# Optimization experiments

Measured on AMD Instinct MI355X. Metric: run time of the kernel, lower is better.

The kernel has to match this reference:

```python
import jax, jax.numpy as jnp
import numpy as np

ITERS = 2
EPS = 1e-6

_OFFSETS = [(a, b, c) for a in (-1, 0, 1) for b in (-1, 0, 1) for c in (-1, 0, 1)]


def _erosion_step(im):
    # product over full 3x3x3 neighborhood (connectivity=26 -> all 27 voxels),
    # out-of-bounds padded with 1 (identity for product)
    B, C, D, H, W = im.shape
    p = jnp.pad(im, ((0, 0), (0, 0), (1, 1), (1, 1), (1, 1)), constant_values=1.0)
    prod = jnp.ones_like(im)
    for dz, dy, dx in _OFFSETS:
        prod = prod * p[:, :, 1 + dz:1 + dz + D, 1 + dy:1 + dy + H, 1 + dx:1 + dx + W]
    return prod


def _distance_map(im, iters=ITERS):
    # PositiveDistanceMap: dils = -SoftErosion3D(1-im) where SoftErosion3D
    # returns temp = -sum_k im_k (im_0 = 1-im, im_{k+1} = im_k * erosion(im_k))
    cur = 1.0 - im
    acc = jnp.zeros_like(cur)
    for _ in range(iters):
        acc = acc + cur
        cur = cur * _erosion_step(cur)
    return acc


def _lah_loss(x, y_onehot):
    axes = (2, 3, 4)  # batch_lah=False -> per (batch, class) reduction
    dm_hat = _distance_map(x)
    dm_gt = _distance_map(y_onehot)
    fp = (dm_gt * x).sum(axes)
    fn = (dm_hat * y_onehot).sum(axes)
    # norm == 0
    fp = fp / (x.sum(axes) + EPS)
    fn = fn / (y_onehot.sum(axes) + EPS)
    lah = (fp + fn + jnp.abs(fp - fn)) / 2  # logsum2 == elementwise max
    return lah[:, 1:].mean()  # do_bg=False drops background channel


def setup_inputs() -> dict:
    key = jax.random.key(0)
    k1, k2 = jax.random.split(key)
    x = jax.random.uniform(k1, (2, 4, 128, 128, 128), dtype=jnp.float32)
    y = jax.random.randint(k2, (2, 1, 128, 128, 128), 0, 4, dtype=jnp.int64)
    return {"x": x, "y": y}


def reference(x, y):
    C = x.shape[1]
    y_onehot = jax.nn.one_hot(y[:, 0], C, axis=1, dtype=x.dtype)  # [B,C,D,H,W]
    return _lah_loss(x, y_onehot)
```

## Files before the change

kernel.cpp:

```cpp
#include <hip/hip_runtime.h>

constexpr int SPB = 1 << 21;
constexpr float EPSV = 1e-6f;

__device__ unsigned char g_mask[2 * SPB];

constexpr int K0_ZSEG = 4;
constexpr int K0_NBLK = (2 * (128 / K0_ZSEG) * 128) / 4;

struct MEnt { int pk, cx, cy; };

__device__ __forceinline__ MEnt k0_load(const int* __restrict__ yb, int s,
                                        int rbase0, bool ym1, bool yp1) {
    MEnt e;
    const int rb = (s << 14) | rbase0;
    int2 vc = *(const int2*)(yb + rb);
    int nib0 = 1 << vc.x, nib1 = 1 << vc.y;
    if (ym1) { int2 vm = *(const int2*)(yb + rb - 128); nib0 |= 1 << vm.x; nib1 |= 1 << vm.y; }
    if (yp1) { int2 vp = *(const int2*)(yb + rb + 128); nib0 |= 1 << vp.x; nib1 |= 1 << vp.y; }
    e.pk = nib0 | (nib1 << 8);
    e.cx = vc.x; e.cy = vc.y;
    return e;
}

__global__ __launch_bounds__(256) void mask_build(const int* __restrict__ y32) {
    const int wid = (blockIdx.x << 2) | (threadIdx.x >> 6);
    const int lane = threadIdx.x & 63;
    const int yy = wid & 127;
    const int zs = (wid >> 7) & 31;
    const int b = (wid >> 12) & 1;
    const int x0 = lane << 1;
    const int z0 = zs * K0_ZSEG;
    const bool ym1 = yy > 0, yp1 = yy < 127;
    const int rbase0 = (yy << 7) | x0;

    const int* __restrict__ yb = y32 + ((long)b << 21);
    unsigned char* __restrict__ mb = g_mask + ((long)b << 21);

    MEnt e0, e1;
    if (z0 > 0) e0 = k0_load(yb, z0 - 1, rbase0, ym1, yp1);
    else { e0.pk = 0; e0.cx = 0; e0.cy = 0; }
    e1 = k0_load(yb, z0, rbase0, ym1, yp1);

#pragma unroll
    for (int dz = 0; dz < K0_ZSEG; ++dz) {
        const int z = z0 + dz;
        MEnt e2;
        if (z + 1 < 128) e2 = k0_load(yb, z + 1, rbase0, ym1, yp1);
        else { e2.pk = 0; e2.cx = 0; e2.cy = 0; }

        const int zor = e0.pk | e1.pk | e2.pk;
        int orL = __shfl_up(zor, 1);
        if (lane == 0) orL = 0;
        int orR = __shfl_down(zor, 1);
        if (lane == 63) orR = 0;
        const int full0 = (zor | (zor >> 8) | (orL >> 8)) & 15;
        const int full1 = (zor | (zor >> 8) | orR) & 15;

        const unsigned short st =
            (unsigned short)((full0 | (e1.cx << 4)) | ((full1 | (e1.cy << 4)) << 8));
        *(unsigned short*)(mb + ((z << 14) | rbase0)) = st;

        e0 = e1; e1 = e2;
    }
}

constexpr int ZC = 8;
constexpr int NBLK = 8 * 16 * (128 / ZC);

__global__ __launch_bounds__(256) void lah_main(const float* __restrict__ x,
                                                float* __restrict__ ws) {
    __shared__ float lds[4][2][4][128];
    __shared__ float sred[4];

    float* acc = ws;
    const float* zp = ws + 64;

    const int bid = blockIdx.x;
    const int plane = bid & 7;
    const int b = plane >> 2, cls = plane & 3;
    const int inner = bid >> 3;
    const int quad = inner & 15;
    const int zq = inner >> 4;
    const int t = threadIdx.x;
    const int w = t >> 6;
    const int rp = quad * 4 + w;
    const int lane = t & 63;
    const int hf = lane >> 5;
    const int lx = lane & 31;
    const int xc = lx << 2;
    const int z0 = zq * ZC;

    const int rowA = 2 * rp - 1 + hf;
    const int rowB = 2 * rp + 1 + hf;
    const int rout = 2 * rp + hf;
    const bool okA = rowA >= 0;
    const bool okB = rowB <= 127;
    const int offA = (rowA << 7) + xc;
    const int offB = (rowB << 7) + xc;

    const float* __restrict__ xp = x + ((long)plane << 21);
    const unsigned char* __restrict__ mb = g_mask + ((long)b << 21);

    auto stage = [&](int k, bool want) {
        const int sl = k & 1;
        const bool kOK = want && ((unsigned)k < 128u);
        const float* pa = (kOK && okA) ? (xp + (k << 14) + offA) : zp;
        const float* pb = (kOK && okB) ? (xp + (k << 14) + offB) : zp;
        __builtin_amdgcn_global_load_lds(
            (const __attribute__((address_space(1))) void*)pa,
            (__attribute__((address_space(3))) void*)&lds[w][sl][0][0], 16, 0, 0);
        __builtin_amdgcn_global_load_lds(
            (const __attribute__((address_space(1))) void*)pb,
            (__attribute__((address_space(3))) void*)&lds[w][sl][2][0], 16, 0, 0);
    };
    auto lmask = [&](int k) -> unsigned {
        const int kc = k < 127 ? k : 127;
        return *(const unsigned*)(mb + (kc << 14) + (rout << 7) + xc);
    };
    auto yprod = [&](int sl, float4& cx) -> float4 {
        const float4 a = *(const float4*)&lds[w][sl][hf][xc];
        const float4 bq = *(const float4*)&lds[w][sl][hf + 1][xc];
        const float4 c = *(const float4*)&lds[w][sl][hf + 2][xc];
        cx = bq;
        float4 o;
        o.x = (1.f - a.x) * (1.f - bq.x) * (1.f - c.x);
        o.y = (1.f - a.y) * (1.f - bq.y) * (1.f - c.y);
        o.z = (1.f - a.z) * (1.f - bq.z) * (1.f - c.z);
        o.w = (1.f - a.w) * (1.f - bq.w) * (1.f - c.w);
        return o;
    };

    stage(z0 - 1, true);
    stage(z0, true);
    asm volatile("s_waitcnt vmcnt(0)" ::: "memory");
    float4 cxd, cx0;
    float4 ypm1 = yprod(1, cxd);
    float4 yp0 = yprod(0, cx0);
    asm volatile("s_waitcnt lgkmcnt(0)" ::: "memory");
    stage(z0 + 1, true);
    unsigned mcur = lmask(z0);

    float fp = 0.f, fn = 0.f, sx = 0.f, sy = 0.f;

#pragma unroll
    for (int dz = 0; dz < ZC; ++dz) {
        const int z = z0 + dz;

        stage(z + 2, dz < ZC - 1);
        const unsigned mnext = lmask(z + 1);

        asm volatile("s_waitcnt vmcnt(3)" ::: "memory");

        float4 cx1;
        const float4 ypp1 = yprod((z + 1) & 1, cx1);

        {
            const float zp0 = ypm1.x * yp0.x * ypp1.x;
            const float zp1 = ypm1.y * yp0.y * ypp1.y;
            const float zp2 = ypm1.z * yp0.z * ypp1.z;
            const float zp3 = ypm1.w * yp0.w * ypp1.w;
            float zl = __shfl_up(zp3, 1);
            if (lx == 0) zl = 1.f;
            float zr = __shfl_down(zp0, 1);
            if (lx == 31) zr = 1.f;
            const float t01 = zp0 * zp1, t12 = zp1 * zp2, t23 = zp2 * zp3;
            const float P[4] = {zl * t01, t01 * zp2, t12 * zp3, t23 * zr};
            const float xa[4] = {cx0.x, cx0.y, cx0.z, cx0.w};
#pragma unroll
            for (int j = 0; j < 4; ++j) {
                const int m = (mcur >> (j * 8)) & 0xFF;
                const bool pres = (m >> cls) & 1;
                const bool eq = (m >> 4) == cls;
                const float xv = xa[j];
                sx += xv;
                fp += eq ? 0.f : xv * (pres ? 1.f : 2.f);
                fn += eq ? (1.f - xv) * (1.f + P[j]) : 0.f;
                sy += eq ? 1.f : 0.f;
            }
        }

        ypm1 = yp0; yp0 = ypp1; cx0 = cx1; mcur = mnext;
    }

    float rr4[4] = {fp, fn, sx, sy};
#pragma unroll
    for (int i = 0; i < 4; ++i) {
        float vv = rr4[i];
#pragma unroll
        for (int off = 32; off >= 1; off >>= 1) vv += __shfl_down(vv, off);
        rr4[i] = vv;
    }
    if (t < 4) sred[t] = 0.f;
    __syncthreads();
    if (lane == 0) {
#pragma unroll
        for (int i = 0; i < 4; ++i) atomicAdd(&sred[i], rr4[i]);
    }
    __syncthreads();
    if (t < 4)
        atomicAdd(&acc[b * 16 + t * 4 + cls], sred[t]);
}

__global__ void lah_finalize(const float* __restrict__ acc, float* __restrict__ out) {
    float loss = 0.f;
#pragma unroll
    for (int b = 0; b < 2; ++b) {
#pragma unroll
        for (int c = 1; c < 4; ++c) {
            const float fp = acc[b * 16 + 0 + c];
            const float fn = acc[b * 16 + 4 + c];
            const float sxv = acc[b * 16 + 8 + c];
            const float syv = acc[b * 16 + 12 + c];
            loss += fmaxf(fp / (sxv + EPSV), fn / (syv + EPSV));
        }
    }
    out[0] = loss / 6.f;
}

extern "C" void kernel_launch(void* const* d_in, const int* in_sizes, int n_in,
                              void* d_out, int out_size, void* d_ws, size_t ws_size,
                              hipStream_t stream) {
    const float* x = (const float*)d_in[0];
    const int* y32 = (const int*)d_in[1];
    float* out = (float*)d_out;
    float* ws = (float*)d_ws;

    hipMemsetAsync(d_ws, 0, 4096, stream);
    mask_build<<<K0_NBLK, 256, 0, stream>>>(y32);
    lah_main<<<NBLK, 256, 0, stream>>>(x, ws);
    lah_finalize<<<1, 1, 0, stream>>>(ws, out);
}
```

Measured before the change: 47.41 us.

## Split fused 3D product stencil into separable XY pass and Z pass kernels

Replaces the single fused kernel, which staged x rows through LDS and computed the 27-point product in one sweep, with two kernels. The first computes the x- and y-direction partial products per z-slice and writes them to a workspace buffer. The second reads that buffer along z, takes the z product, and accumulates the loss terms. This removes the LDS staging and redundant row products, but adds a full 64 MB intermediate write and read through global memory.

```diff
diff --git a/kernel.cpp b/kernel.cpp
--- a/kernel.cpp
+++ b/kernel.cpp
@@ -65,122 +65,110 @@
     }
 }
 
-constexpr int ZC = 8;
-constexpr int NBLK = 8 * 16 * (128 / ZC);
-
-__global__ __launch_bounds__(256) void lah_main(const float* __restrict__ x,
-                                                float* __restrict__ ws) {
-    __shared__ float lds[4][2][4][128];
+constexpr int P12_NBLK = 2048;
+
+__global__ __launch_bounds__(256) void pass12(const float* __restrict__ x,
+                                              float* __restrict__ ws) {
+    float* __restrict__ py = ws + 1024;
+    const int bid = blockIdx.x;
+    const int plane = bid & 7;
+    const int inner = bid >> 3;
+    const int z = inner & 127;
+    const int half = inner >> 7;
+    const int w = threadIdx.x >> 6;
+    const int lane = threadIdx.x & 63;
+    const int y0 = (half * 4 + w) << 4;
+    const int xo = lane << 1;
+
+    const float* __restrict__ xs = x + ((long)plane << 21) + (z << 14) + xo;
+    float* __restrict__ ps = py + ((long)plane << 21) + (z << 14) + xo;
+
+    auto xprow = [&](int y) -> float2 {
+        if ((unsigned)y > 127u) return make_float2(1.f, 1.f);
+        const float2 v = *(const float2*)(xs + (y << 7));
+        const float a0 = 1.f - v.x, a1 = 1.f - v.y;
+        float lft = __shfl_up(a1, 1); if (lane == 0) lft = 1.f;
+        float rgt = __shfl_down(a0, 1); if (lane == 63) rgt = 1.f;
+        const float c = a0 * a1;
+        return make_float2(lft * c, c * rgt);
+    };
+
+    float2 r0 = xprow(y0 - 1);
+    float2 r1 = xprow(y0);
+#pragma unroll
+    for (int dy = 0; dy < 16; ++dy) {
+        const int y = y0 + dy;
+        const float2 r2 = xprow(y + 1);
+        *(float2*)(ps + (y << 7)) =
+            make_float2(r0.x * r1.x * r2.x, r0.y * r1.y * r2.y);
+        r0 = r1; r1 = r2;
+    }
+}
+
+constexpr int P3_NBLK = 2048;
+
+__global__ __launch_bounds__(256) void pass3(const float* __restrict__ x,
+                                             float* __restrict__ ws) {
+    float* __restrict__ acc = ws;
+    const float* __restrict__ py = ws + 1024;
     __shared__ float sred[4];
-
-    float* acc = ws;
-    const float* zp = ws + 64;
 
     const int bid = blockIdx.x;
     const int plane = bid & 7;
     const int b = plane >> 2, cls = plane & 3;
     const int inner = bid >> 3;
-    const int quad = inner & 15;
-    const int zq = inner >> 4;
+    const int yy = inner & 127;
+    const int half = inner >> 7;
     const int t = threadIdx.x;
     const int w = t >> 6;
-    const int rp = quad * 4 + w;
     const int lane = t & 63;
-    const int hf = lane >> 5;
-    const int lx = lane & 31;
-    const int xc = lx << 2;
-    const int z0 = zq * ZC;
-
-    const int rowA = 2 * rp - 1 + hf;
-    const int rowB = 2 * rp + 1 + hf;
-    const int rout = 2 * rp + hf;
-    const bool okA = rowA >= 0;
-    const bool okB = rowB <= 127;
-    const int offA = (rowA << 7) + xc;
-    const int offB = (rowB << 7) + xc;
-
-    const float* __restrict__ xp = x + ((long)plane << 21);
-    const unsigned char* __restrict__ mb = g_mask + ((long)b << 21);
-
-    auto stage = [&](int k, bool want) {
-        const int sl = k & 1;
-        const bool kOK = want && ((unsigned)k < 128u);
-        const float* pa = (kOK && okA) ? (xp + (k << 14) + offA) : zp;
-        const float* pb = (kOK && okB) ? (xp + (k << 14) + offB) : zp;
-        __builtin_amdgcn_global_load_lds(
-            (const __attribute__((address_space(1))) void*)pa,
-            (__attribute__((address_space(3))) void*)&lds[w][sl][0][0], 16, 0, 0);
-        __builtin_amdgcn_global_load_lds(
-            (const __attribute__((address_space(1))) void*)pb,
-            (__attribute__((address_space(3))) void*)&lds[w][sl][2][0], 16, 0, 0);
+    const int z0 = ((half * 4 + w) << 4);
+    const int xo = lane << 1;
+
+    const long pb = (long)plane << 21;
+    const float* __restrict__ xs = x + pb + (yy << 7) + xo;
+    const float* __restrict__ ps = py + pb + (yy << 7) + xo;
+    const unsigned char* __restrict__ ms = g_mask + ((long)b << 21) + (yy << 7) + xo;
+
+    auto pyrow = [&](int z) -> float2 {
+        if ((unsigned)z > 127u) return make_float2(1.f, 1.f);
+        return *(const float2*)(ps + (z << 14));
     };
-    auto lmask = [&](int k) -> unsigned {
-        const int kc = k < 127 ? k : 127;
-        return *(const unsigned*)(mb + (kc << 14) + (rout << 7) + xc);
-    };
-    auto yprod = [&](int sl, float4& cx) -> float4 {
-        const float4 a = *(const float4*)&lds[w][sl][hf][xc];
-        const float4 bq = *(const float4*)&lds[w][sl][hf + 1][xc];
-        const float4 c = *(const float4*)&lds[w][sl][hf + 2][xc];
-        cx = bq;
-        float4 o;
-        o.x = (1.f - a.x) * (1.f - bq.x) * (1.f - c.x);
-        o.y = (1.f - a.y) * (1.f - bq.y) * (1.f - c.y);
-        o.z = (1.f - a.z) * (1.f - bq.z) * (1.f - c.z);
-        o.w = (1.f - a.w) * (1.f - bq.w) * (1.f - c.w);
-        return o;
-    };
-
-    stage(z0 - 1, true);
-    stage(z0, true);
-    asm volatile("s_waitcnt vmcnt(0)" ::: "memory");
-    float4 cxd, cx0;
-    float4 ypm1 = yprod(1, cxd);
-    float4 yp0 = yprod(0, cx0);
-    asm volatile("s_waitcnt lgkmcnt(0)" ::: "memory");
-    stage(z0 + 1, true);
-    unsigned mcur = lmask(z0);
 
     float fp = 0.f, fn = 0.f, sx = 0.f, sy = 0.f;
 
-#pragma unroll
-    for (int dz = 0; dz < ZC; ++dz) {
+    float2 r0 = pyrow(z0 - 1);
+    float2 r1 = pyrow(z0);
+#pragma unroll
+    for (int dz = 0; dz < 16; ++dz) {
         const int z = z0 + dz;
-
-        stage(z + 2, dz < ZC - 1);
-        const unsigned mnext = lmask(z + 1);
-
-        asm volatile("s_waitcnt vmcnt(3)" ::: "memory");
-
-        float4 cx1;
-        const float4 ypp1 = yprod((z + 1) & 1, cx1);
+        const float2 r2 = pyrow(z + 1);
+        const float2 xv = *(const float2*)(xs + (z << 14));
+        const unsigned m2 = *(const unsigned short*)(ms + (z << 14));
+
+        const float P0 = r0.x * r1.x * r2.x;
+        const float P1 = r0.y * r1.y * r2.y;
 
         {
-            const float zp0 = ypm1.x * yp0.x * ypp1.x;
-            const float zp1 = ypm1.y * yp0.y * ypp1.y;
-            const float zp2 = ypm1.z * yp0.z * ypp1.z;
-            const float zp3 = ypm1.w * yp0.w * ypp1.w;
-            float zl = __shfl_up(zp3, 1);
-            if (lx == 0) zl = 1.f;
-            float zr = __shfl_down(zp0, 1);
-            if (lx == 31) zr = 1.f;
-            const float t01 = zp0 * zp1, t12 = zp1 * zp2, t23 = zp2 * zp3;
-            const float P[4] = {zl * t01, t01 * zp2, t12 * zp3, t23 * zr};
-            const float xa[4] = {cx0.x, cx0.y, cx0.z, cx0.w};
-#pragma unroll
-            for (int j = 0; j < 4; ++j) {
-                const int m = (mcur >> (j * 8)) & 0xFF;
-                const bool pres = (m >> cls) & 1;
-                const bool eq = (m >> 4) == cls;
-                const float xv = xa[j];
-                sx += xv;
-                fp += eq ? 0.f : xv * (pres ? 1.f : 2.f);
-                fn += eq ? (1.f - xv) * (1.f + P[j]) : 0.f;
-                sy += eq ? 1.f : 0.f;
-            }
+            const int m = m2 & 0xFF;
+            const bool pres = (m >> cls) & 1;
+            const bool eq = (m >> 4) == cls;
+            sx += xv.x;
+            fp += eq ? 0.f : xv.x * (pres ? 1.f : 2.f);
+            fn += eq ? (1.f - xv.x) * (1.f + P0) : 0.f;
+            sy += eq ? 1.f : 0.f;
         }
-
-        ypm1 = yp0; yp0 = ypp1; cx0 = cx1; mcur = mnext;
+        {
+            const int m = (m2 >> 8) & 0xFF;
+            const bool pres = (m >> cls) & 1;
+            const bool eq = (m >> 4) == cls;
+            sx += xv.y;
+            fp += eq ? 0.f : xv.y * (pres ? 1.f : 2.f);
+            fn += eq ? (1.f - xv.y) * (1.f + P1) : 0.f;
+            sy += eq ? 1.f : 0.f;
+        }
+
+        r0 = r1; r1 = r2;
     }
 
     float rr4[4] = {fp, fn, sx, sy};
@@ -228,6 +216,7 @@
 
     hipMemsetAsync(d_ws, 0, 4096, stream);
     mask_build<<<K0_NBLK, 256, 0, stream>>>(y32);
-    lah_main<<<NBLK, 256, 0, stream>>>(x, ws);
+    pass12<<<P12_NBLK, 256, 0, stream>>>(x, ws);
+    pass3<<<P3_NBLK, 256, 0, stream>>>(x, ws);
     lah_finalize<<<1, 1, 0, stream>>>(ws, out);
 }
```

After: 67.70 us. +42.8%, slower.
